# Kernel tuning notes

Measured on AMD Instinct MI355X. Metric: run time of the kernel, lower is better.

The kernel has to match this reference:

```python
import jax, jax.numpy as jnp
import numpy as np

B, N, DIN, DOUT = 32, 1024, 256, 256


def setup_inputs() -> dict:
    key = jax.random.key(0)
    ks = jax.random.split(key, 7)
    s = 1.0 / np.sqrt(DIN)
    return {
        "x": jax.random.normal(ks[0], (B, N, DIN), dtype=jnp.float32),
        "Wq": jax.random.uniform(ks[1], (DOUT, DIN), minval=-s, maxval=s, dtype=jnp.float32),
        "bq": jax.random.uniform(ks[2], (DOUT,), minval=-s, maxval=s, dtype=jnp.float32),
        "Wk": jax.random.uniform(ks[3], (DOUT, DIN), minval=-s, maxval=s, dtype=jnp.float32),
        "bk": jax.random.uniform(ks[4], (DOUT,), minval=-s, maxval=s, dtype=jnp.float32),
        "Wv": jax.random.uniform(ks[5], (DOUT, DIN), minval=-s, maxval=s, dtype=jnp.float32),
        "bv": jax.random.uniform(ks[6], (DOUT,), minval=-s, maxval=s, dtype=jnp.float32),
    }


def reference(x, Wq, bq, Wk, bk, Wv, bv):
    # q, k, v: (B, N, Dout)
    q = jnp.einsum("bnd,od->bno", x, Wq) + bq
    k = jnp.einsum("bnd,od->bno", x, Wk) + bk
    v = jnp.einsum("bnd,od->bno", x, Wv) + bv
    # logits: (B, N, N) = q @ k^T per batch
    logits = jnp.einsum("bnd,bmd->bnm", q, k)
    # NOTE: softmax over the BATCH dim (axis=0), as in the original module
    attn = jax.nn.softmax(logits, axis=0)
    out = jnp.einsum("bnm,bmd->bnd", attn, v)  # (B, N, Dout)
    return out
```

## Files before the change

kernel.cpp:

```cpp
#include <hip/hip_runtime.h>

typedef __bf16 bf16x8 __attribute__((ext_vector_type(8)));
typedef __bf16 bf16x4 __attribute__((ext_vector_type(4)));
typedef float  f32x4  __attribute__((ext_vector_type(4)));

#define BK 64

__device__ __forceinline__ void g2l16(const void* g, void* l) {
    __builtin_amdgcn_global_load_lds((const __attribute__((address_space(1))) void*)g,
                                     (__attribute__((address_space(3))) void*)l, 16, 0, 0);
}


__global__ __launch_bounds__(256)
void gemm_proj(const __bf16* __restrict__ A, const __bf16* __restrict__ Wb,
               __bf16* __restrict__ qkv, const float* __restrict__ bpack)
{
    __shared__ __align__(16) __bf16 smem[128 * 128];
    __bf16* As = smem;
    __bf16* Bs = smem + 128 * BK;

    const int tid  = threadIdx.x;
    const int w    = tid >> 6;
    const int lane = tid & 63;
    const int quad = lane >> 4;
    const int l16  = lane & 15;
    const int wm   = w & 1;
    const int wn   = w >> 1;

    const int m0 = blockIdx.x * 128;
    const int n0 = blockIdx.y * 128;
    const int z  = blockIdx.z;

    const __bf16* Bb   = Wb + (size_t)z * 131072;
    const float*  bias = bpack + z * 256;

    const int srow = (w << 3) + (lane >> 3);
    const int scol = ((lane & 7) ^ (lane >> 3)) << 3;
    char* ldsA = (char*)As + (size_t)w * 1024;
    char* ldsB = (char*)Bs + (size_t)w * 1024;

    const __bf16* Ag = A  + (size_t)(m0 + srow) * 256 + scol;
    const __bf16* Bg = Bb + (size_t)(n0 + srow) * 256 + scol;

    f32x4 acc[4][4] = {};

    for (int k0 = 0; k0 < 256; k0 += BK) {
        __syncthreads();
        #pragma unroll
        for (int c = 0; c < 4; c++)
            g2l16(Ag + (size_t)(c * 32) * 256 + k0, ldsA + c * 4096);
        #pragma unroll
        for (int c = 0; c < 4; c++)
            g2l16(Bg + (size_t)(c * 32) * 256 + k0, ldsB + c * 4096);
        __syncthreads();

        #pragma unroll
        for (int kk = 0; kk < BK; kk += 32) {
            const int ub = kk >> 3;
            bf16x8 a[4], b[4];
            #pragma unroll
            for (int mt = 0; mt < 4; mt++) {
                const int row = wm * 64 + mt * 16 + l16;
                const int cp  = ((quad + ub) ^ (row & 7)) << 3;
                a[mt] = *(const bf16x8*)&As[row * BK + cp];
            }
            #pragma unroll
            for (int nt = 0; nt < 4; nt++) {
                const int row = wn * 64 + nt * 16 + l16;
                const int cp  = ((quad + ub) ^ (row & 7)) << 3;
                b[nt] = *(const bf16x8*)&Bs[row * BK + cp];
            }
            #pragma unroll
            for (int mt = 0; mt < 4; mt++)
                #pragma unroll
                for (int nt = 0; nt < 4; nt++)
                    acc[mt][nt] = __builtin_amdgcn_mfma_f32_16x16x32_bf16(
                        a[mt], b[nt], acc[mt][nt], 0, 0, 0);
        }
    }

    __syncthreads();
    if (z < 2) {
        #pragma unroll
        for (int mt = 0; mt < 4; mt++) {
            const int rl = wm * 64 + mt * 16 + quad * 4;
            #pragma unroll
            for (int nt = 0; nt < 4; nt++) {
                const int cl = wn * 64 + nt * 16 + l16;
                const float bn = bias[n0 + cl];
                #pragma unroll
                for (int r = 0; r < 4; r++) {
                    const int row = rl + r;
                    smem[row * 128 + ((((cl >> 3) ^ (row & 7)) << 3) | (cl & 7))] =
                        (__bf16)(acc[mt][nt][r] + bn);
                }
            }
        }
        __syncthreads();
        __bf16* C = qkv + (size_t)z * 8388608;
        #pragma unroll
        for (int i = 0; i < 8; i++) {
            const int c   = tid + i * 256;
            const int row = c >> 4, u = c & 15;
            *(bf16x8*)&C[(size_t)(m0 + row) * 256 + n0 + u * 8] =
                *(const bf16x8*)&smem[row * 128 + ((u ^ (row & 7)) << 3)];
        }
    } else {
        #pragma unroll
        for (int mt = 0; mt < 4; mt++) {
            const int ml = wm * 64 + mt * 16 + quad * 4;
            #pragma unroll
            for (int nt = 0; nt < 4; nt++) {
                const int dl = wn * 64 + nt * 16 + l16;
                const float bn = bias[n0 + dl];
                bf16x4 pk;
                #pragma unroll
                for (int r = 0; r < 4; r++) pk[r] = (__bf16)(acc[mt][nt][r] + bn);
                *(bf16x4*)&smem[dl * 128 + ((((ml >> 3) ^ (dl & 7)) << 3) | (ml & 7))] = pk;
            }
        }
        __syncthreads();
        __bf16* C = qkv + 2 * 8388608;
        const int bidx = m0 >> 10, mbase = m0 & 1023;
        #pragma unroll
        for (int i = 0; i < 8; i++) {
            const int c  = tid + i * 256;
            const int dl = c >> 4, u = c & 15;
            *(bf16x8*)&C[(size_t)bidx * 262144 + (size_t)(n0 + dl) * 1024 + mbase + u * 8] =
                *(const bf16x8*)&smem[dl * 128 + ((u ^ (dl & 7)) << 3)];
        }
    }
}

__global__ __launch_bounds__(256)
void gemm_logits(const __bf16* __restrict__ Q, const __bf16* __restrict__ Km,
                 __bf16* __restrict__ E)
{
    __shared__ __align__(16) __bf16 smem[128 * 128];
    __bf16* As = smem;
    __bf16* Bs = smem + 128 * BK;

    const int tid  = threadIdx.x;
    const int w    = tid >> 6;
    const int lane = tid & 63;
    const int quad = lane >> 4;
    const int l16  = lane & 15;
    const int wm   = w & 1;
    const int wn   = w >> 1;

    const int id = blockIdx.x;
    const int x  = id & 7, s = id >> 3;
    const int z  = x + ((s >> 6) << 3);
    const int t  = s & 63;
    const int m0 = (t & 7) * 128;
    const int n0 = (t >> 3) * 128;

    const __bf16* Ab = Q  + (size_t)z * 262144;
    const __bf16* Bb = Km + (size_t)z * 262144;

    const int srow = (w << 3) + (lane >> 3);
    const int scol = ((lane & 7) ^ (lane >> 3)) << 3;
    char* ldsA = (char*)As + (size_t)w * 1024;
    char* ldsB = (char*)Bs + (size_t)w * 1024;

    const __bf16* Ag = Ab + (size_t)(m0 + srow) * 256 + scol;
    const __bf16* Bg = Bb + (size_t)(n0 + srow) * 256 + scol;

    f32x4 acc[4][4] = {};

    for (int k0 = 0; k0 < 256; k0 += BK) {
        __syncthreads();
        #pragma unroll
        for (int c = 0; c < 4; c++)
            g2l16(Ag + (size_t)(c * 32) * 256 + k0, ldsA + c * 4096);
        #pragma unroll
        for (int c = 0; c < 4; c++)
            g2l16(Bg + (size_t)(c * 32) * 256 + k0, ldsB + c * 4096);
        __syncthreads();

        #pragma unroll
        for (int kk = 0; kk < BK; kk += 32) {
            const int ub = kk >> 3;
            bf16x8 a[4], b[4];
            #pragma unroll
            for (int mt = 0; mt < 4; mt++) {
                const int row = wm * 64 + mt * 16 + l16;
                const int cp  = ((quad + ub) ^ (row & 7)) << 3;
                a[mt] = *(const bf16x8*)&As[row * BK + cp];
            }
            #pragma unroll
            for (int nt = 0; nt < 4; nt++) {
                const int row = wn * 64 + nt * 16 + l16;
                const int cp  = ((quad + ub) ^ (row & 7)) << 3;
                b[nt] = *(const bf16x8*)&Bs[row * BK + cp];
            }
            #pragma unroll
            for (int mt = 0; mt < 4; mt++)
                #pragma unroll
                for (int nt = 0; nt < 4; nt++)
                    acc[mt][nt] = __builtin_amdgcn_mfma_f32_16x16x32_bf16(
                        a[mt], b[nt], acc[mt][nt], 0, 0, 0);
        }
    }

    __syncthreads();
    #pragma unroll
    for (int mt = 0; mt < 4; mt++) {
        const int rl = wm * 64 + mt * 16 + quad * 4;
        #pragma unroll
        for (int nt = 0; nt < 4; nt++) {
            const int cl = wn * 64 + nt * 16 + l16;
            #pragma unroll
            for (int r = 0; r < 4; r++) {
                const int row = rl + r;
                smem[row * 128 + ((((cl >> 3) ^ (row & 7)) << 3) | (cl & 7))] =
                    (__bf16)__expf(acc[mt][nt][r]);
            }
        }
    }
    __syncthreads();
    __bf16* C = E + (size_t)z * 1048576;
    #pragma unroll
    for (int i = 0; i < 8; i++) {
        const int c   = tid + i * 256;
        const int row = c >> 4, u = c & 15;
        *(bf16x8*)&C[(size_t)(m0 + row) * 1024 + n0 + u * 8] =
            *(const bf16x8*)&smem[row * 128 + ((u ^ (row & 7)) << 3)];
    }
}

__global__ __launch_bounds__(256)
void sum_rcp(const __bf16* __restrict__ E, __bf16* __restrict__ rcpS)
{
    const size_t p = (size_t)blockIdx.x * 256 + threadIdx.x;
    const bf16x8* E8 = (const bf16x8*)E;
    float s[8] = {0.f, 0.f, 0.f, 0.f, 0.f, 0.f, 0.f, 0.f};
    #pragma unroll
    for (int b = 0; b < 32; b++) {
        const bf16x8 e = E8[(size_t)b * 131072 + p];
        #pragma unroll
        for (int j = 0; j < 8; j++) s[j] += (float)e[j];
    }
    bf16x8 o;
    #pragma unroll
    for (int j = 0; j < 8; j++) o[j] = (__bf16)__builtin_amdgcn_rcpf(s[j]);
    ((bf16x8*)rcpS)[p] = o;
}

__global__ __launch_bounds__(256)
void gemm_pv(const __bf16* __restrict__ E, const __bf16* __restrict__ rcpS,
             const __bf16* __restrict__ vT, float* __restrict__ out)
{
    __shared__ __align__(16) __bf16 As[128 * BK];
    __shared__ __align__(16) __bf16 Bs[64 * BK];

    const int tid  = threadIdx.x;
    const int w    = tid >> 6;
    const int lane = tid & 63;
    const int quad = lane >> 4;
    const int l16  = lane & 15;
    const int wm   = w & 1;
    const int wn   = w >> 1;

    const int id = blockIdx.x;
    const int x  = id & 7, s = id >> 3;
    const int z  = x + ((s >> 5) << 3);
    const int t  = s & 31;
    const int m0 = (t & 7) * 128;
    const int n0 = (t >> 3) * 64;

    const __bf16* Eb = E  + (size_t)z * 1048576;
    const __bf16* Vb = vT + (size_t)z * 262144;
    float*        Ob = out + (size_t)z * 262144;

    const int srow = (w << 3) + (lane >> 3);
    const int scol = ((lane & 7) ^ (lane >> 3)) << 3;
    char* ldsAw = (char*)As + w * 1024 + lane * 16;
    char* ldsB  = (char*)Bs + (size_t)w * 1024;

    const __bf16* Ag = Eb   + (size_t)(m0 + srow) * 1024 + scol;
    const __bf16* Rg = rcpS + (size_t)(m0 + srow) * 1024 + scol;
    const __bf16* Bg = Vb   + (size_t)(n0 + srow) * 1024 + scol;

    f32x4 acc[4][2] = {};

    for (int k0 = 0; k0 < 1024; k0 += BK) {
        __syncthreads();
        #pragma unroll
        for (int c = 0; c < 4; c++) {
            const bf16x8 e  = *(const bf16x8*)(Ag + (size_t)(c * 32) * 1024 + k0);
            const bf16x8 rs = *(const bf16x8*)(Rg + (size_t)(c * 32) * 1024 + k0);
            bf16x8 o;
            #pragma unroll
            for (int j = 0; j < 8; j++) o[j] = (__bf16)((float)e[j] * (float)rs[j]);
            *(bf16x8*)(ldsAw + c * 4096) = o;
        }
        #pragma unroll
        for (int c = 0; c < 2; c++)
            g2l16(Bg + (size_t)(c * 32) * 1024 + k0, ldsB + c * 4096);
        __syncthreads();

        #pragma unroll
        for (int kk = 0; kk < BK; kk += 32) {
            const int ub = kk >> 3;
            bf16x8 a[4], b[2];
            #pragma unroll
            for (int mt = 0; mt < 4; mt++) {
                const int row = wm * 64 + mt * 16 + l16;
                const int cp  = ((quad + ub) ^ (row & 7)) << 3;
                a[mt] = *(const bf16x8*)&As[row * BK + cp];
            }
            #pragma unroll
            for (int nt = 0; nt < 2; nt++) {
                const int row = wn * 32 + nt * 16 + l16;
                const int cp  = ((quad + ub) ^ (row & 7)) << 3;
                b[nt] = *(const bf16x8*)&Bs[row * BK + cp];
            }
            #pragma unroll
            for (int mt = 0; mt < 4; mt++)
                #pragma unroll
                for (int nt = 0; nt < 2; nt++)
                    acc[mt][nt] = __builtin_amdgcn_mfma_f32_16x16x32_bf16(
                        a[mt], b[nt], acc[mt][nt], 0, 0, 0);
        }
    }

    #pragma unroll
    for (int mt = 0; mt < 4; mt++) {
        const int mb = m0 + wm * 64 + mt * 16 + quad * 4;
        #pragma unroll
        for (int nt = 0; nt < 2; nt++) {
            const int n = n0 + wn * 32 + nt * 16 + l16;
            #pragma unroll
            for (int r = 0; r < 4; r++)
                Ob[(size_t)(mb + r) * 256 + n] = acc[mt][nt][r];
        }
    }
}

__global__ __launch_bounds__(256)
void cvt_all(const float* __restrict__ x,
             const float* __restrict__ Wq, const float* __restrict__ Wk,
             const float* __restrict__ Wv,
             const float* __restrict__ bq, const float* __restrict__ bk,
             const float* __restrict__ bv,
             __bf16* __restrict__ xb, __bf16* __restrict__ Wqb,
             float* __restrict__ bpack)
{
    const int i = blockIdx.x * 256 + threadIdx.x;
    if (i < 1073152) {
        const float* s; __bf16* d; int off;
        if (i < 1048576)      { s = x;  d = xb;            off = i; }
        else if (i < 1056768) { s = Wq; d = Wqb;           off = i - 1048576; }
        else if (i < 1064960) { s = Wk; d = Wqb + 131072;  off = i - 1056768; }
        else                  { s = Wv; d = Wqb + 262144;  off = i - 1064960; }
        const float4* s4 = (const float4*)s;
        const float4 f0 = s4[off * 2], f1 = s4[off * 2 + 1];
        bf16x8 o;
        o[0] = (__bf16)f0.x; o[1] = (__bf16)f0.y; o[2] = (__bf16)f0.z; o[3] = (__bf16)f0.w;
        o[4] = (__bf16)f1.x; o[5] = (__bf16)f1.y; o[6] = (__bf16)f1.z; o[7] = (__bf16)f1.w;
        ((bf16x8*)d)[off] = o;
    } else if (i < 1073344) {
        const int j = i - 1073152;
        const int sel = j >> 6, jj = j & 63;
        const float* s = sel == 0 ? bq : (sel == 1 ? bk : bv);
        ((float4*)bpack)[j] = ((const float4*)s)[jj];
    }
}

extern "C" void kernel_launch(void* const* d_in, const int* in_sizes, int n_in,
                              void* d_out, int out_size, void* d_ws, size_t ws_size,
                              hipStream_t stream)
{
    const float* x  = (const float*)d_in[0];
    const float* Wq = (const float*)d_in[1];
    const float* bq = (const float*)d_in[2];
    const float* Wk = (const float*)d_in[3];
    const float* bk = (const float*)d_in[4];
    const float* Wv = (const float*)d_in[5];
    const float* bv = (const float*)d_in[6];
    float* out = (float*)d_out;

    char* ws = (char*)d_ws;
    __bf16* rcpS = (__bf16*)ws;
    __bf16* xb   = (__bf16*)(ws + (2u  << 20));
    __bf16* qkv  = (__bf16*)(ws + (18u << 20));
    __bf16* E    = (__bf16*)(ws + (66u << 20));
    __bf16* Wqb  = (__bf16*)(ws + (130u << 20));
    float*  bpack = (float*)(ws + (130u << 20) + (1u << 20));

    cvt_all<<<4194, 256, 0, stream>>>(x, Wq, Wk, Wv, bq, bk, bv, xb, Wqb, bpack);

    gemm_proj<<<dim3(256, 2, 3), 256, 0, stream>>>(xb, Wqb, qkv, bpack);

    gemm_logits<<<2048, 256, 0, stream>>>(qkv, qkv + 8388608, E);

    sum_rcp<<<512, 256, 0, stream>>>(E, rcpS);

    gemm_pv<<<1024, 256, 0, stream>>>(E, rcpS, qkv + 2 * 8388608, out);
}
```

Measured before the change: 197.4 us.

## Triple-buffer LDS pipelines in logits and PV GEMMs, halve logits N tile

Both gemm_logits and gemm_pv now use a three-stage LDS ring with explicit vmcnt waits and a single barrier per k-step, so global loads for later tiles overlap MFMA work on the current tile. gemm_pv also prefetches E and rcpS into registers two steps ahead and writes the scaled A tile one step ahead. gemm_logits moves from 128x128 to 128x64 tiles, doubling the grid to 4096 blocks. This adds LDS use per block (72KB) and register pressure, which may lower occupancy, and the hand-written waitcnt logic is fragile.

```diff
diff --git a/kernel.cpp b/kernel.cpp
--- a/kernel.cpp
+++ b/kernel.cpp
@@ -137,9 +137,7 @@
 void gemm_logits(const __bf16* __restrict__ Q, const __bf16* __restrict__ Km,
                  __bf16* __restrict__ E)
 {
-    __shared__ __align__(16) __bf16 smem[128 * 128];
-    __bf16* As = smem;
-    __bf16* Bs = smem + 128 * BK;
+    __shared__ __align__(16) __bf16 smem[3 * 12288];
 
     const int tid  = threadIdx.x;
     const int w    = tid >> 6;
@@ -151,38 +149,49 @@
 
     const int id = blockIdx.x;
     const int x  = id & 7, s = id >> 3;
-    const int z  = x + ((s >> 6) << 3);
-    const int t  = s & 63;
-    const int m0 = (t & 7) * 128;
-    const int n0 = (t >> 3) * 128;
+    const int z  = x + ((s >> 7) << 3);
+    const int t_ = s & 127;
+    const int m0 = (t_ & 7) * 128;
+    const int n0 = (t_ >> 3) * 64;
 
     const __bf16* Ab = Q  + (size_t)z * 262144;
     const __bf16* Bb = Km + (size_t)z * 262144;
 
     const int srow = (w << 3) + (lane >> 3);
     const int scol = ((lane & 7) ^ (lane >> 3)) << 3;
-    char* ldsA = (char*)As + (size_t)w * 1024;
-    char* ldsB = (char*)Bs + (size_t)w * 1024;
 
     const __bf16* Ag = Ab + (size_t)(m0 + srow) * 256 + scol;
     const __bf16* Bg = Bb + (size_t)(n0 + srow) * 256 + scol;
 
-    f32x4 acc[4][4] = {};
-
-    for (int k0 = 0; k0 < 256; k0 += BK) {
-        __syncthreads();
+    f32x4 acc[4][2] = {};
+
+    auto STAGE = [&](int buf, int k0) {
+        char* base = (char*)smem + buf * 24576;
         #pragma unroll
         for (int c = 0; c < 4; c++)
-            g2l16(Ag + (size_t)(c * 32) * 256 + k0, ldsA + c * 4096);
-        #pragma unroll
-        for (int c = 0; c < 4; c++)
-            g2l16(Bg + (size_t)(c * 32) * 256 + k0, ldsB + c * 4096);
-        __syncthreads();
-
+            g2l16(Ag + (size_t)(c * 32) * 256 + k0, base + w * 1024 + c * 4096);
+        #pragma unroll
+        for (int c = 0; c < 2; c++)
+            g2l16(Bg + (size_t)(c * 32) * 256 + k0, base + 16384 + w * 1024 + c * 4096);
+    };
+
+    STAGE(0, 0);
+    STAGE(1, 64);
+
+    for (int t = 0; t < 4; t++) {
+        if (t < 3) asm volatile("s_waitcnt vmcnt(6)" ::: "memory");
+        else       asm volatile("s_waitcnt vmcnt(0)" ::: "memory");
+        __builtin_amdgcn_sched_barrier(0);
+        __builtin_amdgcn_s_barrier();
+
+        if (t < 2) STAGE((t + 2) % 3, (t + 2) * BK);
+
+        const __bf16* As = smem + (t % 3) * 12288;
+        const __bf16* Bs = As + 8192;
         #pragma unroll
         for (int kk = 0; kk < BK; kk += 32) {
             const int ub = kk >> 3;
-            bf16x8 a[4], b[4];
+            bf16x8 a[4], b[2];
             #pragma unroll
             for (int mt = 0; mt < 4; mt++) {
                 const int row = wm * 64 + mt * 16 + l16;
@@ -190,15 +199,15 @@
                 a[mt] = *(const bf16x8*)&As[row * BK + cp];
             }
             #pragma unroll
-            for (int nt = 0; nt < 4; nt++) {
-                const int row = wn * 64 + nt * 16 + l16;
+            for (int nt = 0; nt < 2; nt++) {
+                const int row = wn * 32 + nt * 16 + l16;
                 const int cp  = ((quad + ub) ^ (row & 7)) << 3;
                 b[nt] = *(const bf16x8*)&Bs[row * BK + cp];
             }
             #pragma unroll
             for (int mt = 0; mt < 4; mt++)
                 #pragma unroll
-                for (int nt = 0; nt < 4; nt++)
+                for (int nt = 0; nt < 2; nt++)
                     acc[mt][nt] = __builtin_amdgcn_mfma_f32_16x16x32_bf16(
                         a[mt], b[nt], acc[mt][nt], 0, 0, 0);
         }
@@ -209,12 +218,12 @@
     for (int mt = 0; mt < 4; mt++) {
         const int rl = wm * 64 + mt * 16 + quad * 4;
         #pragma unroll
-        for (int nt = 0; nt < 4; nt++) {
-            const int cl = wn * 64 + nt * 16 + l16;
+        for (int nt = 0; nt < 2; nt++) {
+            const int cl = wn * 32 + nt * 16 + l16;
             #pragma unroll
             for (int r = 0; r < 4; r++) {
                 const int row = rl + r;
-                smem[row * 128 + ((((cl >> 3) ^ (row & 7)) << 3) | (cl & 7))] =
+                smem[row * 64 + ((((cl >> 3) ^ (row & 7)) << 3) | (cl & 7))] =
                     (__bf16)__expf(acc[mt][nt][r]);
             }
         }
@@ -222,11 +231,11 @@
     __syncthreads();
     __bf16* C = E + (size_t)z * 1048576;
     #pragma unroll
-    for (int i = 0; i < 8; i++) {
+    for (int i = 0; i < 4; i++) {
         const int c   = tid + i * 256;
-        const int row = c >> 4, u = c & 15;
+        const int row = c >> 3, u = c & 7;
         *(bf16x8*)&C[(size_t)(m0 + row) * 1024 + n0 + u * 8] =
-            *(const bf16x8*)&smem[row * 128 + ((u ^ (row & 7)) << 3)];
+            *(const bf16x8*)&smem[row * 64 + ((u ^ (row & 7)) << 3)];
     }
 }
 
@@ -249,11 +258,10 @@
 }
 
 __global__ __launch_bounds__(256)
-void gemm_pv(const __bf16* __restrict__ E, const __bf16* __restrict__ rcpS,
+void gemm_pv(const __bf16* __restrict__ En, const __bf16* __restrict__ rcpS,
              const __bf16* __restrict__ vT, float* __restrict__ out)
 {
-    __shared__ __align__(16) __bf16 As[128 * BK];
-    __shared__ __align__(16) __bf16 Bs[64 * BK];
+    __shared__ __align__(16) __bf16 smem[3 * 12288];
 
     const int tid  = threadIdx.x;
     const int w    = tid >> 6;
@@ -266,41 +274,73 @@
     const int id = blockIdx.x;
     const int x  = id & 7, s = id >> 3;
     const int z  = x + ((s >> 5) << 3);
-    const int t  = s & 31;
-    const int m0 = (t & 7) * 128;
-    const int n0 = (t >> 3) * 64;
-
-    const __bf16* Eb = E  + (size_t)z * 1048576;
+    const int t_ = s & 31;
+    const int m0 = (t_ & 7) * 128;
+    const int n0 = (t_ >> 3) * 64;
+
+    const __bf16* Eb = En + (size_t)z * 1048576;
     const __bf16* Vb = vT + (size_t)z * 262144;
     float*        Ob = out + (size_t)z * 262144;
 
     const int srow = (w << 3) + (lane >> 3);
     const int scol = ((lane & 7) ^ (lane >> 3)) << 3;
-    char* ldsAw = (char*)As + w * 1024 + lane * 16;
-    char* ldsB  = (char*)Bs + (size_t)w * 1024;
 
     const __bf16* Ag = Eb   + (size_t)(m0 + srow) * 1024 + scol;
     const __bf16* Rg = rcpS + (size_t)(m0 + srow) * 1024 + scol;
     const __bf16* Bg = Vb   + (size_t)(n0 + srow) * 1024 + scol;
 
     f32x4 acc[4][2] = {};
-
-    for (int k0 = 0; k0 < 1024; k0 += BK) {
-        __syncthreads();
+    bf16x8 e[4], rs[4];
+
+    auto LOAD_ER = [&](int k0) {
         #pragma unroll
         for (int c = 0; c < 4; c++) {
-            const bf16x8 e  = *(const bf16x8*)(Ag + (size_t)(c * 32) * 1024 + k0);
-            const bf16x8 rs = *(const bf16x8*)(Rg + (size_t)(c * 32) * 1024 + k0);
+            e[c]  = *(const bf16x8*)(Ag + (size_t)(c * 32) * 1024 + k0);
+            rs[c] = *(const bf16x8*)(Rg + (size_t)(c * 32) * 1024 + k0);
+        }
+    };
+    auto G2L_B = [&](int buf, int k0) {
+        char* base = (char*)smem + buf * 24576 + 16384;
+        #pragma unroll
+        for (int c = 0; c < 2; c++)
+            g2l16(Bg + (size_t)(c * 32) * 1024 + k0, base + w * 1024 + c * 4096);
+    };
+    auto WRITE_A = [&](int buf) {
+        char* base = (char*)smem + buf * 24576;
+        #pragma unroll
+        for (int c = 0; c < 4; c++) {
             bf16x8 o;
             #pragma unroll
-            for (int j = 0; j < 8; j++) o[j] = (__bf16)((float)e[j] * (float)rs[j]);
-            *(bf16x8*)(ldsAw + c * 4096) = o;
-        }
-        #pragma unroll
-        for (int c = 0; c < 2; c++)
-            g2l16(Bg + (size_t)(c * 32) * 1024 + k0, ldsB + c * 4096);
-        __syncthreads();
-
+            for (int j = 0; j < 8; j++)
+                o[j] = (__bf16)((float)e[c][j] * (float)rs[c][j]);
+            *(bf16x8*)(base + w * 1024 + lane * 16 + c * 4096) = o;
+        }
+    };
+
+    LOAD_ER(0);
+    G2L_B(0, 0);
+    asm volatile("s_waitcnt vmcnt(2)" ::: "memory");
+    __builtin_amdgcn_sched_barrier(0);
+    WRITE_A(0);
+    LOAD_ER(64);
+    G2L_B(1, 64);
+
+    for (int t = 0; t < 16; t++) {
+        if (t < 15) asm volatile("s_waitcnt vmcnt(2)" ::: "memory");
+        else        asm volatile("s_waitcnt vmcnt(0)" ::: "memory");
+        __builtin_amdgcn_sched_barrier(0);
+        if (t < 15) WRITE_A((t + 1) % 3);
+        asm volatile("s_waitcnt lgkmcnt(0)" ::: "memory");
+        __builtin_amdgcn_sched_barrier(0);
+        __builtin_amdgcn_s_barrier();
+
+        if (t < 14) {
+            LOAD_ER((t + 2) * BK);
+            G2L_B((t + 2) % 3, (t + 2) * BK);
+        }
+
+        const __bf16* As = smem + (t % 3) * 12288;
+        const __bf16* Bs = As + 8192;
         #pragma unroll
         for (int kk = 0; kk < BK; kk += 32) {
             const int ub = kk >> 3;
@@ -394,7 +434,7 @@
 
     gemm_proj<<<dim3(256, 2, 3), 256, 0, stream>>>(xb, Wqb, qkv, bpack);
 
-    gemm_logits<<<2048, 256, 0, stream>>>(qkv, qkv + 8388608, E);
+    gemm_logits<<<4096, 256, 0, stream>>>(qkv, qkv + 8388608, E);
 
     sum_rcp<<<512, 256, 0, stream>>>(E, rcpS);
 
```

After: 197.6 us. No clear change (+0.1%).
